# Kernel tuning notes

Measured on AMD Instinct MI355X. Metric: run time of the kernel, lower is better.

## Reference

```python
import jax, jax.numpy as jnp
import numpy as np

B, S, E, H = 4, 2048, 512, 1024

def setup_inputs() -> dict:
    key = jax.random.key(0)
    ks = jax.random.split(key, 8)
    s = 1.0 / np.sqrt(H)
    return {
        "hidden_states": jax.random.normal(ks[0], (B, S, H), jnp.float32),
        "external_embeddings": jax.random.normal(ks[1], (B, E, H), jnp.float32),
        "Wq": jax.random.normal(ks[2], (H, H), jnp.float32) * s,
        "bq": jax.random.normal(ks[3], (H,), jnp.float32) * 0.02,
        "Wk": jax.random.normal(ks[4], (H, H), jnp.float32) * s,
        "bk": jax.random.normal(ks[5], (H,), jnp.float32) * 0.02,
        "Wv": jax.random.normal(ks[6], (H, H), jnp.float32) * s,
        "bv": jax.random.normal(ks[7], (H,), jnp.float32) * 0.02,
    }

def reference(hidden_states, external_embeddings, Wq, bq, Wk, bk, Wv, bv):
    # Projections (torch Linear semantics: here weights stored as [in,out])
    q = hidden_states @ Wq + bq              # [B,S,H]
    k_tok = hidden_states @ Wk + bk          # [B,S,H]
    v_tok = hidden_states @ Wv + bv          # [B,S,H]
    k_ext = external_embeddings @ Wk + bk    # [B,E,H]
    v_ext = external_embeddings @ Wv + bv    # [B,E,H]
    # Each token attends to [its own key] ++ [external keys]; NO 1/sqrt(d) scaling
    # and NO head splitting, matching the original forward exactly.
    s_self = jnp.einsum('bsh,bsh->bs', q, k_tok)[..., None]   # [B,S,1]
    s_ext = jnp.einsum('bsh,beh->bse', q, k_ext)              # [B,S,E]
    scores = jnp.concatenate([s_self, s_ext], axis=-1)        # [B,S,1+E]
    probs = jax.nn.softmax(scores, axis=-1)
    ctx = probs[..., :1] * v_tok + jnp.einsum('bse,beh->bsh', probs[..., 1:], v_ext)
    return ctx  # [B,S,H]
```

## Files before the change

### kernel.cpp

```cpp
#include <hip/hip_runtime.h>
#include <stdint.h>

#define BB 4
#define SS 2048
#define EE 512
#define HH 1024

typedef _Float16 f16;
typedef __attribute__((ext_vector_type(8))) _Float16 f16x8;
typedef __attribute__((ext_vector_type(4))) _Float16 f16x4;
typedef __attribute__((ext_vector_type(4))) float f32x4;

__device__ __forceinline__ void async16(void* lds, const void* g) {
  __builtin_amdgcn_global_load_lds(
      (const __attribute__((address_space(1))) unsigned int*)g,
      (__attribute__((address_space(3))) unsigned int*)lds, 16, 0, 0);
}

#define MFMA16 __builtin_amdgcn_mfma_f32_16x16x32_f16

__global__ __launch_bounds__(256) void cast_kernel(const float* __restrict__ xh32,
                                                   const float* __restrict__ xe32,
                                                   f16* __restrict__ xh,
                                                   f16* __restrict__ xe) {
  const int i = blockIdx.x * 256 + threadIdx.x;
  const int n4h = 8192 * HH / 4;
  const float* src = i < n4h ? xh32 : xe32;
  f16* dst = i < n4h ? xh : xe;
  const int k = i < n4h ? i : i - n4h;
  const float4 v = ((const float4*)src)[k];
  f16x4 o;
  o.x = (f16)v.x; o.y = (f16)v.y; o.z = (f16)v.z; o.w = (f16)v.w;
  ((f16x4*)dst)[k] = o;
}

__global__ void wsplit_kernel(const float* __restrict__ Wq, const float* __restrict__ Wk,
                              const float* __restrict__ Wv, f16* __restrict__ wt_hi,
                              f16* __restrict__ wt_lo) {
  __shared__ float tile[32][33];
  const int k0 = blockIdx.x * 32;
  const int n0g = blockIdx.y * 32;
  const int which = n0g >> 10;
  const float* W = which == 0 ? Wq : (which == 1 ? Wk : Wv);
  const int n0 = n0g & 1023;
  const int tx = threadIdx.x, ty = threadIdx.y;
#pragma unroll
  for (int i = 0; i < 32; i += 8)
    tile[ty + i][tx] = W[(size_t)(k0 + ty + i) * 1024 + n0 + tx];
  __syncthreads();
#pragma unroll
  for (int i = 0; i < 32; i += 8) {
    const int np = n0g + ty + i;
    const float v = tile[tx][ty + i];
    const size_t idx = (size_t)np * 1024 + k0 + tx;
    const f16 h = (f16)v;
    wt_hi[idx] = h;
    wt_lo[idx] = (f16)(v - (float)h);
  }
}

__global__ __launch_bounds__(512, 2) void proj_kernel(
    const f16* __restrict__ xh, const f16* __restrict__ xe,
    const f16* __restrict__ wt_hi, const f16* __restrict__ wt_lo,
    const float* __restrict__ bq, const float* __restrict__ bk,
    const float* __restrict__ bv, f16* __restrict__ q_hi, f16* __restrict__ q_lo,
    f16* __restrict__ kt, f16* __restrict__ vt,
    f16* __restrict__ ke_hi, f16* __restrict__ ke_lo, f16* __restrict__ veT) {
  const int g = blockIdx.x;
  const int j = g & 7;
  const int s = g >> 3;
  int mrow0, colB0;
  bool ext = false, splitB = false;
  if (s < 20) {
    splitB = true;
    if (s < 16) {
      colB0 = (s >> 2) * 256;
      mrow0 = ((s & 3) * 8 + j) * 256;
    } else {
      ext = true;
      colB0 = 1024 + (s - 16) * 256;
      mrow0 = j * 256;
    }
  } else {
    const int s2 = s - 20;
    if (s2 < 32) {
      colB0 = (4 + (s2 >> 2)) * 256;
      mrow0 = ((s2 & 3) * 8 + j) * 256;
    } else {
      ext = true;
      colB0 = 1024 + (4 + (s2 - 32)) * 256;
      mrow0 = j * 256;
    }
  }
  const int NT = splitB ? 32 : 16;

  __shared__ f16 lds[65536];

  const int tid = threadIdx.x;
  const int wave = tid >> 6, lane = tid & 63;
  const int wm = wave >> 2, wn = wave & 3;
  const int frow = lane & 15, qd = lane >> 4;

  const f16* A0 = (ext ? xe : xh) + (size_t)mrow0 * HH;
  const f16* Bhi = wt_hi + (size_t)colB0 * HH;
  const f16* Blo = wt_lo + (size_t)colB0 * HH;

  const int srow = tid >> 2;
  const int scol = ((tid & 3) ^ ((srow >> 1) & 3)) * 8;
  const size_t gO0 = (size_t)srow * HH + scol;
  const size_t gO1 = (size_t)(128 + srow) * HH + scol;
  const int ldst0 = (wave * 64) * 8;
  const int ldst1 = (512 + wave * 64) * 8;

  int offA[8], offB[4];
#pragma unroll
  for (int i = 0; i < 8; ++i) {
    const int r = wm * 128 + i * 16 + frow;
    offA[i] = r * 32 + ((qd ^ ((r >> 1) & 3)) * 8);
  }
#pragma unroll
  for (int jj = 0; jj < 4; ++jj) {
    const int r = wn * 64 + jj * 16 + frow;
    offB[jj] = r * 32 + ((qd ^ ((r >> 1) & 3)) * 8);
  }

  f32x4 acc[8][4];
#pragma unroll
  for (int i = 0; i < 8; ++i)
#pragma unroll
    for (int jj = 0; jj < 4; ++jj)
#pragma unroll
      for (int r = 0; r < 4; ++r) acc[i][jj][r] = 0.0f;

  {
    f16* dA0 = &lds[0];
    f16* dB0 = &lds[32768];
    f16* dA1 = &lds[8192];
    f16* dB1 = &lds[32768 + 8192];
    async16(&dA0[ldst0], A0 + gO0);       async16(&dA0[ldst1], A0 + gO1);
    async16(&dB0[ldst0], Bhi + gO0);      async16(&dB0[ldst1], Bhi + gO1);
    async16(&dA1[ldst0], A0 + 32 + gO0);  async16(&dA1[ldst1], A0 + 32 + gO1);
    async16(&dB1[ldst0], Bhi + 32 + gO0); async16(&dB1[ldst1], Bhi + 32 + gO1);
  }
  asm volatile("s_waitcnt vmcnt(4)" ::: "memory");
  __builtin_amdgcn_s_barrier();

  for (int t = 0; t < NT; ++t) {
    const int cur = t & 1, nxt = cur ^ 1;
    const bool st = (t + 1 < NT);
    const int kn = ((t + 1) & 15) * 64;
    const f16* An = A0 + kn;
    const f16* Bn = (((t + 1) & 16) ? Blo : Bhi) + kn;
    const f16* lA0 = &lds[(cur * 2 + 0) * 8192];
    const f16* lB0 = &lds[32768 + (cur * 2 + 0) * 8192];
    const f16* lA1 = &lds[(cur * 2 + 1) * 8192];
    const f16* lB1 = &lds[32768 + (cur * 2 + 1) * 8192];
    f16* sA0 = &lds[(nxt * 2 + 0) * 8192];
    f16* sB0 = &lds[32768 + (nxt * 2 + 0) * 8192];
    f16* sA1 = &lds[(nxt * 2 + 1) * 8192];
    f16* sB1 = &lds[32768 + (nxt * 2 + 1) * 8192];

    f16x8 a[8], b0, b1;

#pragma unroll
    for (int i = 0; i < 8; ++i) a[i] = *(const f16x8*)&lA0[offA[i]];
    b0 = *(const f16x8*)&lB0[offB[0]];
    b1 = *(const f16x8*)&lB0[offB[1]];
    if (st) { async16(&sA0[ldst0], An + gO0); async16(&sA0[ldst1], An + gO1); }
    __builtin_amdgcn_s_barrier();
    __builtin_amdgcn_s_setprio(1);
#pragma unroll
    for (int i = 0; i < 8; ++i) {
      acc[i][0] = MFMA16(a[i], b0, acc[i][0], 0, 0, 0);
      acc[i][1] = MFMA16(a[i], b1, acc[i][1], 0, 0, 0);
    }
    __builtin_amdgcn_s_setprio(0);
    __builtin_amdgcn_s_barrier();

    b0 = *(const f16x8*)&lB0[offB[2]];
    b1 = *(const f16x8*)&lB0[offB[3]];
    if (st) { async16(&sB0[ldst0], Bn + gO0); async16(&sB0[ldst1], Bn + gO1); }
    __builtin_amdgcn_s_barrier();
    __builtin_amdgcn_s_setprio(1);
#pragma unroll
    for (int i = 0; i < 8; ++i) {
      acc[i][2] = MFMA16(a[i], b0, acc[i][2], 0, 0, 0);
      acc[i][3] = MFMA16(a[i], b1, acc[i][3], 0, 0, 0);
    }
    __builtin_amdgcn_s_setprio(0);
    if (t == NT - 1) {
      asm volatile("s_waitcnt vmcnt(0)" ::: "memory");
    } else {
      asm volatile("s_waitcnt vmcnt(4)" ::: "memory");
    }
    __builtin_amdgcn_s_barrier();

#pragma unroll
    for (int i = 0; i < 8; ++i) a[i] = *(const f16x8*)&lA1[offA[i]];
    b0 = *(const f16x8*)&lB1[offB[0]];
    b1 = *(const f16x8*)&lB1[offB[1]];
    if (st) { async16(&sA1[ldst0], An + 32 + gO0); async16(&sA1[ldst1], An + 32 + gO1); }
    __builtin_amdgcn_s_barrier();
    __builtin_amdgcn_s_setprio(1);
#pragma unroll
    for (int i = 0; i < 8; ++i) {
      acc[i][0] = MFMA16(a[i], b0, acc[i][0], 0, 0, 0);
      acc[i][1] = MFMA16(a[i], b1, acc[i][1], 0, 0, 0);
    }
    __builtin_amdgcn_s_setprio(0);
    __builtin_amdgcn_s_barrier();

    b0 = *(const f16x8*)&lB1[offB[2]];
    b1 = *(const f16x8*)&lB1[offB[3]];
    if (st) { async16(&sB1[ldst0], Bn + 32 + gO0); async16(&sB1[ldst1], Bn + 32 + gO1); }
    __builtin_amdgcn_s_barrier();
    __builtin_amdgcn_s_setprio(1);
#pragma unroll
    for (int i = 0; i < 8; ++i) {
      acc[i][2] = MFMA16(a[i], b0, acc[i][2], 0, 0, 0);
      acc[i][3] = MFMA16(a[i], b1, acc[i][3], 0, 0, 0);
    }
    __builtin_amdgcn_s_setprio(0);
    asm volatile("s_waitcnt vmcnt(4)" ::: "memory");
    __builtin_amdgcn_s_barrier();
  }

  const int er0 = wm * 128 + qd * 4;
  const int ec0 = wn * 64 + frow;
  float bias[4];
#pragma unroll
  for (int jj = 0; jj < 4; ++jj) {
    const int c = colB0 + ec0 + jj * 16;
    bias[jj] = c < 1024 ? bq[c] : (c < 2048 ? bk[c - 1024] : bv[c - 2048]);
  }

  if (!ext) {
    if (colB0 < 1024) {
#pragma unroll
      for (int jj = 0; jj < 4; ++jj) {
        const int c = colB0 + ec0 + jj * 16;
#pragma unroll
        for (int i = 0; i < 8; ++i)
#pragma unroll
          for (int r = 0; r < 4; ++r) {
            const int row = mrow0 + er0 + i * 16 + r;
            const float val = acc[i][jj][r] + bias[jj];
            const size_t idx = (size_t)row * HH + c;
            const f16 h = (f16)val;
            q_hi[idx] = h;
            q_lo[idx] = (f16)(val - (float)h);
          }
      }
    } else if (colB0 < 2048) {
#pragma unroll
      for (int jj = 0; jj < 4; ++jj) {
        const int c = colB0 + ec0 + jj * 16 - 1024;
#pragma unroll
        for (int i = 0; i < 8; ++i)
#pragma unroll
          for (int r = 0; r < 4; ++r) {
            const int row = mrow0 + er0 + i * 16 + r;
            kt[(size_t)row * HH + c] = (f16)(acc[i][jj][r] + bias[jj]);
          }
      }
    } else {
#pragma unroll
      for (int jj = 0; jj < 4; ++jj) {
        const int c = colB0 + ec0 + jj * 16 - 2048;
#pragma unroll
        for (int i = 0; i < 8; ++i)
#pragma unroll
          for (int r = 0; r < 4; ++r) {
            const int row = mrow0 + er0 + i * 16 + r;
            vt[(size_t)row * HH + c] = (f16)(acc[i][jj][r] + bias[jj]);
          }
      }
    }
  } else {
    if (colB0 < 2048) {
#pragma unroll
      for (int jj = 0; jj < 4; ++jj) {
        const int c = colB0 + ec0 + jj * 16 - 1024;
#pragma unroll
        for (int i = 0; i < 8; ++i)
#pragma unroll
          for (int r = 0; r < 4; ++r) {
            const int row = mrow0 + er0 + i * 16 + r;
            const float val = acc[i][jj][r] + bias[jj];
            const size_t idx = (size_t)row * HH + c;
            const f16 h = (f16)val;
            ke_hi[idx] = h;
            ke_lo[idx] = (f16)(val - (float)h);
          }
      }
    } else {
      f16* tl = lds;
      const int b = mrow0 >> 9, e0 = mrow0 & 511;
      const int h0 = colB0 - 2048;
#pragma unroll
      for (int p = 0; p < 2; ++p) {
        __syncthreads();
        if ((wn >> 1) == p) {
          const int hL = (wn & 1) * 64 + frow;
#pragma unroll
          for (int jj = 0; jj < 4; ++jj)
#pragma unroll
            for (int i = 0; i < 8; ++i)
#pragma unroll
              for (int r = 0; r < 4; ++r) {
                const int e = er0 + i * 16 + r;
                tl[(hL + jj * 16) * 264 + e] = (f16)(acc[i][jj][r] + bias[jj]);
              }
        }
        __syncthreads();
        for (int c = tid; c < 128 * 32; c += 512) {
          const int hL = c >> 5, ch = c & 31;
          const f16x8 v = *(const f16x8*)&tl[hL * 264 + ch * 8];
          *(f16x8*)&veT[(size_t)(b * HH + h0 + p * 128 + hL) * EE + e0 + ch * 8] = v;
        }
      }
    }
  }
}

__global__ __launch_bounds__(512, 1) void score_kernel(
    const f16* __restrict__ q_hi, const f16* __restrict__ q_lo,
    const f16* __restrict__ ke_hi, const f16* __restrict__ ke_lo,
    float* __restrict__ s_part) {
  const int b = blockIdx.z & 3;
  const int khalf = blockIdx.z >> 2;
  const int mtile = blockIdx.y;
  const int ntile = blockIdx.x;

  __shared__ f16 lds[73728];

  const int tid = threadIdx.x;
  const int wave = tid >> 6, lane = tid & 63;
  const int wm = wave >> 1, wn = wave & 1;
  const int frow = lane & 15, qd = lane >> 4;

  const size_t aoff = ((size_t)b * SS + mtile * 256) * HH + khalf * 512;
  const size_t boff = ((size_t)b * EE + ntile * 128) * HH + khalf * 512;
  const f16* Ah = q_hi + aoff;
  const f16* Al = q_lo + aoff;
  const f16* Bh = ke_hi + boff;
  const f16* Bl = ke_lo + boff;

  const int srow = tid >> 2;
  const int scol = ((tid & 3) ^ ((srow >> 1) & 3)) * 8;
  const size_t gA0 = (size_t)srow * HH + scol;
  const size_t gA1 = (size_t)(128 + srow) * HH + scol;
  const int ldstA0 = (wave * 64) * 8;
  const int ldstA1 = (512 + wave * 64) * 8;
  const int ldstB0 = (wave * 64) * 8;

  int offA[4], offB[4];
#pragma unroll
  for (int i = 0; i < 4; ++i) {
    const int r = wm * 64 + i * 16 + frow;
    offA[i] = r * 32 + ((qd ^ ((r >> 1) & 3)) * 8);
  }
#pragma unroll
  for (int jj = 0; jj < 4; ++jj) {
    const int r = wn * 64 + jj * 16 + frow;
    offB[jj] = r * 32 + ((qd ^ ((r >> 1) & 3)) * 8);
  }

  f32x4 acc[4][4];
#pragma unroll
  for (int i = 0; i < 4; ++i)
#pragma unroll
    for (int jj = 0; jj < 4; ++jj)
#pragma unroll
      for (int r = 0; r < 4; ++r) acc[i][jj][r] = 0.0f;

#pragma unroll
  for (int p = 0; p < 2; ++p) {
    f16* dAh = &lds[p * 24576];
    f16* dAl = &lds[p * 24576 + 8192];
    f16* dBh = &lds[p * 24576 + 16384];
    f16* dBl = &lds[p * 24576 + 20480];
    const int ko = p * 32;
    async16(&dAh[ldstA0], Ah + ko + gA0); async16(&dAh[ldstA1], Ah + ko + gA1);
    async16(&dBh[ldstB0], Bh + ko + gA0);
    async16(&dBl[ldstB0], Bl + ko + gA0);
    async16(&dAl[ldstA0], Al + ko + gA0); async16(&dAl[ldstA1], Al + ko + gA1);
  }
  asm volatile("s_waitcnt vmcnt(6)" ::: "memory");
  __builtin_amdgcn_s_barrier();

  int cur = 0, stg = 2;
  for (int t = 0; t < 16; ++t) {
    const bool st = (t < 14);
    const int kk = (t + 2) * 32;
    const f16* lAh = &lds[cur * 24576];
    const f16* lAl = &lds[cur * 24576 + 8192];
    const f16* lBh = &lds[cur * 24576 + 16384];
    const f16* lBl = &lds[cur * 24576 + 20480];
    f16* sAh = &lds[stg * 24576];
    f16* sAl = &lds[stg * 24576 + 8192];
    f16* sBh = &lds[stg * 24576 + 16384];
    f16* sBl = &lds[stg * 24576 + 20480];

    f16x8 ah[4], bh[4], x[4];

#pragma unroll
    for (int i = 0; i < 4; ++i) ah[i] = *(const f16x8*)&lAh[offA[i]];
#pragma unroll
    for (int jj = 0; jj < 4; ++jj) bh[jj] = *(const f16x8*)&lBh[offB[jj]];
    if (st) {
      async16(&sAh[ldstA0], Ah + kk + gA0); async16(&sAh[ldstA1], Ah + kk + gA1);
    }
    __builtin_amdgcn_s_barrier();
    __builtin_amdgcn_s_setprio(1);
#pragma unroll
    for (int i = 0; i < 4; ++i)
#pragma unroll
      for (int jj = 0; jj < 4; ++jj)
        acc[i][jj] = MFMA16(ah[i], bh[jj], acc[i][jj], 0, 0, 0);
    __builtin_amdgcn_s_setprio(0);
    __builtin_amdgcn_s_barrier();

#pragma unroll
    for (int jj = 0; jj < 4; ++jj) x[jj] = *(const f16x8*)&lBl[offB[jj]];
    if (st) {
      async16(&sBh[ldstB0], Bh + kk + gA0);
      async16(&sBl[ldstB0], Bl + kk + gA0);
    }
    __builtin_amdgcn_s_barrier();
    __builtin_amdgcn_s_setprio(1);
#pragma unroll
    for (int i = 0; i < 4; ++i)
#pragma unroll
      for (int jj = 0; jj < 4; ++jj)
        acc[i][jj] = MFMA16(ah[i], x[jj], acc[i][jj], 0, 0, 0);
    __builtin_amdgcn_s_setprio(0);
    __builtin_amdgcn_s_barrier();

#pragma unroll
    for (int i = 0; i < 4; ++i) x[i] = *(const f16x8*)&lAl[offA[i]];
    if (st) {
      async16(&sAl[ldstA0], Al + kk + gA0); async16(&sAl[ldstA1], Al + kk + gA1);
    }
    __builtin_amdgcn_s_barrier();
    __builtin_amdgcn_s_setprio(1);
#pragma unroll
    for (int i = 0; i < 4; ++i)
#pragma unroll
      for (int jj = 0; jj < 4; ++jj)
        acc[i][jj] = MFMA16(x[i], bh[jj], acc[i][jj], 0, 0, 0);
    __builtin_amdgcn_s_setprio(0);
    if (t < 14)       { asm volatile("s_waitcnt vmcnt(6)" ::: "memory"); }
    else if (t == 14) { asm volatile("s_waitcnt vmcnt(0)" ::: "memory"); }
    __builtin_amdgcn_s_barrier();

    cur = (cur == 2) ? 0 : cur + 1;
    stg = (stg == 2) ? 0 : stg + 1;
  }

  float* dst = s_part + (size_t)khalf * BB * SS * EE + (size_t)b * SS * EE;
#pragma unroll
  for (int jj = 0; jj < 4; ++jj) {
    const int e = ntile * 128 + wn * 64 + jj * 16 + frow;
#pragma unroll
    for (int i = 0; i < 4; ++i)
#pragma unroll
      for (int r = 0; r < 4; ++r) {
        const int s = mtile * 256 + wm * 64 + i * 16 + qd * 4 + r;
        dst[(size_t)s * EE + e] = acc[i][jj][r];
      }
  }
}

__global__ __launch_bounds__(256) void softmax_kernel(
    const f16* __restrict__ q_hi, const f16* __restrict__ q_lo,
    const f16* __restrict__ kt, const float* __restrict__ s_part,
    f16* __restrict__ probs, float* __restrict__ p_self) {
  const int t = blockIdx.x * 4 + (threadIdx.x >> 6);
  const int lane = threadIdx.x & 63;

  const size_t base = (size_t)t * HH;
  float ss = 0.f;
#pragma unroll
  for (int it = 0; it < 4; ++it) {
    const int off = it * 256 + lane * 4;
    const f16x4 qh = *(const f16x4*)&q_hi[base + off];
    const f16x4 ql = *(const f16x4*)&q_lo[base + off];
    const f16x4 kh = *(const f16x4*)&kt[base + off];
    ss += ((float)qh.x + (float)ql.x) * (float)kh.x;
    ss += ((float)qh.y + (float)ql.y) * (float)kh.y;
    ss += ((float)qh.z + (float)ql.z) * (float)kh.z;
    ss += ((float)qh.w + (float)ql.w) * (float)kh.w;
  }
#pragma unroll
  for (int m = 32; m > 0; m >>= 1) ss += __shfl_xor(ss, m, 64);

  const float* r0 = s_part + (size_t)t * EE;
  const float* r1 = s_part + (size_t)BB * SS * EE + (size_t)t * EE;
  const float4 a0 = *(const float4*)&r0[lane * 4];
  const float4 a1 = *(const float4*)&r0[256 + lane * 4];
  const float4 c0 = *(const float4*)&r1[lane * 4];
  const float4 c1 = *(const float4*)&r1[256 + lane * 4];
  const float v0x = a0.x + c0.x, v0y = a0.y + c0.y, v0z = a0.z + c0.z, v0w = a0.w + c0.w;
  const float v1x = a1.x + c1.x, v1y = a1.y + c1.y, v1z = a1.z + c1.z, v1w = a1.w + c1.w;
  float m = fmaxf(fmaxf(fmaxf(v0x, v0y), fmaxf(v0z, v0w)),
                  fmaxf(fmaxf(v1x, v1y), fmaxf(v1z, v1w)));
#pragma unroll
  for (int sh = 32; sh > 0; sh >>= 1) m = fmaxf(m, __shfl_xor(m, sh, 64));
  m = fmaxf(m, ss);
  const float e0 = __expf(v0x - m), e1 = __expf(v0y - m);
  const float e2 = __expf(v0z - m), e3 = __expf(v0w - m);
  const float e4 = __expf(v1x - m), e5 = __expf(v1y - m);
  const float e6 = __expf(v1z - m), e7 = __expf(v1w - m);
  float sum = ((e0 + e1) + (e2 + e3)) + ((e4 + e5) + (e6 + e7));
#pragma unroll
  for (int sh = 32; sh > 0; sh >>= 1) sum += __shfl_xor(sum, sh, 64);
  const float es = __expf(ss - m);
  const float inv = 1.0f / (sum + es);
  f16x4 p0, p1;
  p0.x = (f16)(e0 * inv); p0.y = (f16)(e1 * inv);
  p0.z = (f16)(e2 * inv); p0.w = (f16)(e3 * inv);
  p1.x = (f16)(e4 * inv); p1.y = (f16)(e5 * inv);
  p1.z = (f16)(e6 * inv); p1.w = (f16)(e7 * inv);
  *(f16x4*)&probs[(size_t)t * EE + lane * 4] = p0;
  *(f16x4*)&probs[(size_t)t * EE + 256 + lane * 4] = p1;
  if (lane == 0) p_self[t] = es * inv;
}

__global__ __launch_bounds__(512, 2) void pv_kernel(
    const f16* __restrict__ probs, const f16* __restrict__ veT,
    const float* __restrict__ p_self, const f16* __restrict__ vt,
    float* __restrict__ out) {
  const int b = blockIdx.z;
  const int mtile = blockIdx.y;
  const int ntile = blockIdx.x;

  __shared__ f16 lds[36864];

  const int tid = threadIdx.x;
  const int wave = tid >> 6, lane = tid & 63;
  const int wm = wave >> 1, wn = wave & 1;
  const int frow = lane & 15, qd = lane >> 4;

  const size_t aoff = ((size_t)b * SS + mtile * 256) * EE;
  const size_t boff = ((size_t)b * HH + ntile * 128) * EE;
  const f16* A = probs + aoff;
  const f16* Bv = veT + boff;

  const int srow = tid >> 2;
  const int scol = ((tid & 3) ^ ((srow >> 1) & 3)) * 8;
  const size_t gA0 = (size_t)srow * EE + scol;
  const size_t gA1 = (size_t)(128 + srow) * EE + scol;
  const int ldstA0 = (wave * 64) * 8;
  const int ldstA1 = (512 + wave * 64) * 8;
  const int ldstB0 = (wave * 64) * 8;

  int offA[4], offB[4];
#pragma unroll
  for (int i = 0; i < 4; ++i) {
    const int r = wm * 64 + i * 16 + frow;
    offA[i] = r * 32 + ((qd ^ ((r >> 1) & 3)) * 8);
  }
#pragma unroll
  for (int jj = 0; jj < 4; ++jj) {
    const int r = wn * 64 + jj * 16 + frow;
    offB[jj] = r * 32 + ((qd ^ ((r >> 1) & 3)) * 8);
  }

  f32x4 acc[4][4];
#pragma unroll
  for (int i = 0; i < 4; ++i)
#pragma unroll
    for (int jj = 0; jj < 4; ++jj)
#pragma unroll
      for (int r = 0; r < 4; ++r) acc[i][jj][r] = 0.0f;

  {
    f16* dA0 = &lds[0], *dB0 = &lds[8192];
    f16* dA1 = &lds[12288], *dB1 = &lds[12288 + 8192];
    async16(&dA0[ldstA0], A + gA0); async16(&dA0[ldstA1], A + gA1);
    async16(&dB0[ldstB0], Bv + gA0);
    async16(&dA1[ldstA0], A + 32 + gA0); async16(&dA1[ldstA1], A + 32 + gA1);
    async16(&dB1[ldstB0], Bv + 32 + gA0);
  }
  asm volatile("s_waitcnt vmcnt(3)" ::: "memory");
  __builtin_amdgcn_s_barrier();

  int cur = 0, stg = 2;
  for (int t = 0; t < 16; ++t) {
    const bool st = (t < 14);
    const int kk = (t + 2) * 32;
    const f16* lA = &lds[cur * 12288];
    const f16* lB = &lds[cur * 12288 + 8192];
    f16* sA = &lds[stg * 12288];
    f16* sB = &lds[stg * 12288 + 8192];

    f16x8 a[4], b[4];

#pragma unroll
    for (int i = 0; i < 4; ++i) a[i] = *(const f16x8*)&lA[offA[i]];
    b[0] = *(const f16x8*)&lB[offB[0]];
    b[1] = *(const f16x8*)&lB[offB[1]];
    if (st) { async16(&sA[ldstA0], A + kk + gA0); async16(&sA[ldstA1], A + kk + gA1); }
    __builtin_amdgcn_s_barrier();
    __builtin_amdgcn_s_setprio(1);
#pragma unroll
    for (int i = 0; i < 4; ++i) {
      acc[i][0] = MFMA16(a[i], b[0], acc[i][0], 0, 0, 0);
      acc[i][1] = MFMA16(a[i], b[1], acc[i][1], 0, 0, 0);
    }
    __builtin_amdgcn_s_setprio(0);
    __builtin_amdgcn_s_barrier();

    b[2] = *(const f16x8*)&lB[offB[2]];
    b[3] = *(const f16x8*)&lB[offB[3]];
    if (st) async16(&sB[ldstB0], Bv + kk + gA0);
    __builtin_amdgcn_s_barrier();
    __builtin_amdgcn_s_setprio(1);
#pragma unroll
    for (int i = 0; i < 4; ++i) {
      acc[i][2] = MFMA16(a[i], b[2], acc[i][2], 0, 0, 0);
      acc[i][3] = MFMA16(a[i], b[3], acc[i][3], 0, 0, 0);
    }
    __builtin_amdgcn_s_setprio(0);
    if (t < 14)      { asm volatile("s_waitcnt vmcnt(3)" ::: "memory"); }
    else if (t == 14){ asm volatile("s_waitcnt vmcnt(0)" ::: "memory"); }
    __builtin_amdgcn_s_barrier();

    cur = (cur == 2) ? 0 : cur + 1;
    stg = (stg == 2) ? 0 : stg + 1;
  }

#pragma unroll
  for (int jj = 0; jj < 4; ++jj) {
    const int h = ntile * 128 + wn * 64 + jj * 16 + frow;
#pragma unroll
    for (int i = 0; i < 4; ++i)
#pragma unroll
      for (int r = 0; r < 4; ++r) {
        const int s = mtile * 256 + wm * 64 + i * 16 + qd * 4 + r;
        const size_t t = (size_t)b * SS + s;
        __builtin_nontemporal_store(
            acc[i][jj][r] + p_self[t] * (float)vt[t * HH + h], &out[t * HH + h]);
      }
  }
}

extern "C" void kernel_launch(void* const* d_in, const int* in_sizes, int n_in,
                              void* d_out, int out_size, void* d_ws, size_t ws_size,
                              hipStream_t stream) {
  const float* hidden = (const float*)d_in[0];
  const float* ext    = (const float*)d_in[1];
  const float* Wq = (const float*)d_in[2];
  const float* bq = (const float*)d_in[3];
  const float* Wk = (const float*)d_in[4];
  const float* bk = (const float*)d_in[5];
  const float* Wv = (const float*)d_in[6];
  const float* bv = (const float*)d_in[7];
  float* out = (float*)d_out;

  char* ws = (char*)d_ws;
  size_t off = 0;
  auto alloc = [&](size_t bytes) {
    char* p = ws + off;
    off += (bytes + 255) & ~(size_t)255;
    return p;
  };
  const size_t TOK = 8192, EXT = 2048;
  f16* xh    = (f16*)alloc(TOK * HH * 2);
  f16* xe    = (f16*)alloc(EXT * HH * 2);
  f16* wt_hi = (f16*)alloc(3072ull * HH * 2);
  f16* wt_lo = (f16*)alloc(3072ull * HH * 2);
  f16* q_hi  = (f16*)alloc(TOK * HH * 2);
  f16* q_lo  = (f16*)alloc(TOK * HH * 2);
  f16* kt    = (f16*)alloc(TOK * HH * 2);
  f16* vt    = (f16*)alloc(TOK * HH * 2);
  f16* ke_hi = (f16*)alloc(EXT * HH * 2);
  f16* ke_lo = (f16*)alloc(EXT * HH * 2);
  f16* veT   = (f16*)alloc((size_t)BB * HH * EE * 2);
  float* p_self = (float*)alloc(TOK * 4);
  float* s_part = (float*)alloc(2ull * BB * SS * EE * 4);
  f16* probs    = (f16*)alloc((size_t)BB * SS * EE * 2);

  cast_kernel<<<10240, 256, 0, stream>>>(hidden, ext, xh, xe);
  wsplit_kernel<<<dim3(32, 96), dim3(32, 8), 0, stream>>>(Wq, Wk, Wv, wt_hi, wt_lo);

  proj_kernel<<<448, 512, 0, stream>>>(
      xh, xe, wt_hi, wt_lo, bq, bk, bv,
      q_hi, q_lo, kt, vt, ke_hi, ke_lo, veT);

  score_kernel<<<dim3(4, 8, 8), 512, 0, stream>>>(q_hi, q_lo, ke_hi, ke_lo, s_part);
  softmax_kernel<<<2048, 256, 0, stream>>>(q_hi, q_lo, kt, s_part, probs, p_self);
  pv_kernel<<<dim3(8, 8, 4), 512, 0, stream>>>(probs, veT, p_self, vt, out);
}
```

Before: 282.8 us.

## Merge prep kernels and simplify projection GEMM pipeline to smaller K-steps

Fuses the input cast kernel and the weight split/transpose kernel into one launch, removing one kernel launch. The projection GEMM now uses a 32-wide K-step with a plain double buffer: one async prefetch per iteration, a vmcnt(0) wait and one barrier, replacing the four-phase 64-wide schedule with many barriers. LDS use is halved, launch bounds are raised to 4 blocks per CU, and the veT transpose epilogue is reworked to fit the smaller LDS. In exchange it waits for each load to fully drain every step, and the tighter register budget risks spilling the 128-float accumulator.

```diff
diff --git a/kernel.cpp b/kernel.cpp
--- a/kernel.cpp
+++ b/kernel.cpp
@@ -19,47 +19,49 @@
 
 #define MFMA16 __builtin_amdgcn_mfma_f32_16x16x32_f16
 
-__global__ __launch_bounds__(256) void cast_kernel(const float* __restrict__ xh32,
-                                                   const float* __restrict__ xe32,
-                                                   f16* __restrict__ xh,
-                                                   f16* __restrict__ xe) {
-  const int i = blockIdx.x * 256 + threadIdx.x;
-  const int n4h = 8192 * HH / 4;
-  const float* src = i < n4h ? xh32 : xe32;
-  f16* dst = i < n4h ? xh : xe;
-  const int k = i < n4h ? i : i - n4h;
-  const float4 v = ((const float4*)src)[k];
-  f16x4 o;
-  o.x = (f16)v.x; o.y = (f16)v.y; o.z = (f16)v.z; o.w = (f16)v.w;
-  ((f16x4*)dst)[k] = o;
+__global__ __launch_bounds__(256) void prep_kernel(
+    const float* __restrict__ xh32, const float* __restrict__ xe32,
+    const float* __restrict__ Wq, const float* __restrict__ Wk,
+    const float* __restrict__ Wv,
+    f16* __restrict__ xh, f16* __restrict__ xe,
+    f16* __restrict__ wt_hi, f16* __restrict__ wt_lo) {
+  __shared__ float tile[32][33];
+  const int bid = blockIdx.x;
+  if (bid < 10240) {
+    const int i = bid * 256 + threadIdx.x;
+    const int n4h = 8192 * HH / 4;
+    const float* src = i < n4h ? xh32 : xe32;
+    f16* dst = i < n4h ? xh : xe;
+    const int k = i < n4h ? i : i - n4h;
+    const float4 v = ((const float4*)src)[k];
+    f16x4 o;
+    o.x = (f16)v.x; o.y = (f16)v.y; o.z = (f16)v.z; o.w = (f16)v.w;
+    ((f16x4*)dst)[k] = o;
+  } else {
+    const int b2 = bid - 10240;
+    const int k0 = (b2 & 31) * 32;
+    const int n0g = (b2 >> 5) * 32;
+    const int which = n0g >> 10;
+    const float* W = which == 0 ? Wq : (which == 1 ? Wk : Wv);
+    const int n0 = n0g & 1023;
+    const int tx = threadIdx.x & 31, ty = threadIdx.x >> 5;
+#pragma unroll
+    for (int i = 0; i < 32; i += 8)
+      tile[ty + i][tx] = W[(size_t)(k0 + ty + i) * 1024 + n0 + tx];
+    __syncthreads();
+#pragma unroll
+    for (int i = 0; i < 32; i += 8) {
+      const int np = n0g + ty + i;
+      const float v = tile[tx][ty + i];
+      const size_t idx = (size_t)np * 1024 + k0 + tx;
+      const f16 h = (f16)v;
+      wt_hi[idx] = h;
+      wt_lo[idx] = (f16)(v - (float)h);
+    }
+  }
 }
 
-__global__ void wsplit_kernel(const float* __restrict__ Wq, const float* __restrict__ Wk,
-                              const float* __restrict__ Wv, f16* __restrict__ wt_hi,
-                              f16* __restrict__ wt_lo) {
-  __shared__ float tile[32][33];
-  const int k0 = blockIdx.x * 32;
-  const int n0g = blockIdx.y * 32;
-  const int which = n0g >> 10;
-  const float* W = which == 0 ? Wq : (which == 1 ? Wk : Wv);
-  const int n0 = n0g & 1023;
-  const int tx = threadIdx.x, ty = threadIdx.y;
-#pragma unroll
-  for (int i = 0; i < 32; i += 8)
-    tile[ty + i][tx] = W[(size_t)(k0 + ty + i) * 1024 + n0 + tx];
-  __syncthreads();
-#pragma unroll
-  for (int i = 0; i < 32; i += 8) {
-    const int np = n0g + ty + i;
-    const float v = tile[tx][ty + i];
-    const size_t idx = (size_t)np * 1024 + k0 + tx;
-    const f16 h = (f16)v;
-    wt_hi[idx] = h;
-    wt_lo[idx] = (f16)(v - (float)h);
-  }
-}
-
-__global__ __launch_bounds__(512, 2) void proj_kernel(
+__global__ __launch_bounds__(512, 4) void proj_kernel(
     const f16* __restrict__ xh, const f16* __restrict__ xe,
     const f16* __restrict__ wt_hi, const f16* __restrict__ wt_lo,
     const float* __restrict__ bq, const float* __restrict__ bk,
@@ -92,9 +94,9 @@
       mrow0 = j * 256;
     }
   }
-  const int NT = splitB ? 32 : 16;
-
-  __shared__ f16 lds[65536];
+  const int NT = splitB ? 64 : 32;
+
+  __shared__ f16 lds[32768];
 
   const int tid = threadIdx.x;
   const int wave = tid >> 6, lane = tid & 63;
@@ -109,8 +111,8 @@
   const int scol = ((tid & 3) ^ ((srow >> 1) & 3)) * 8;
   const size_t gO0 = (size_t)srow * HH + scol;
   const size_t gO1 = (size_t)(128 + srow) * HH + scol;
-  const int ldst0 = (wave * 64) * 8;
-  const int ldst1 = (512 + wave * 64) * 8;
+  const int ldst0 = wave * 512;
+  const int ldst1 = 4096 + wave * 512;
 
   int offA[8], offB[4];
 #pragma unroll
@@ -132,42 +134,32 @@
 #pragma unroll
       for (int r = 0; r < 4; ++r) acc[i][jj][r] = 0.0f;
 
-  {
-    f16* dA0 = &lds[0];
-    f16* dB0 = &lds[32768];
-    f16* dA1 = &lds[8192];
-    f16* dB1 = &lds[32768 + 8192];
-    async16(&dA0[ldst0], A0 + gO0);       async16(&dA0[ldst1], A0 + gO1);
-    async16(&dB0[ldst0], Bhi + gO0);      async16(&dB0[ldst1], Bhi + gO1);
-    async16(&dA1[ldst0], A0 + 32 + gO0);  async16(&dA1[ldst1], A0 + 32 + gO1);
-    async16(&dB1[ldst0], Bhi + 32 + gO0); async16(&dB1[ldst1], Bhi + 32 + gO1);
-  }
-  asm volatile("s_waitcnt vmcnt(4)" ::: "memory");
+  async16(&lds[ldst0], A0 + gO0);        async16(&lds[ldst1], A0 + gO1);
+  async16(&lds[8192 + ldst0], Bhi + gO0); async16(&lds[8192 + ldst1], Bhi + gO1);
+  asm volatile("s_waitcnt vmcnt(0)" ::: "memory");
   __builtin_amdgcn_s_barrier();
 
   for (int t = 0; t < NT; ++t) {
     const int cur = t & 1, nxt = cur ^ 1;
-    const bool st = (t + 1 < NT);
-    const int kn = ((t + 1) & 15) * 64;
-    const f16* An = A0 + kn;
-    const f16* Bn = (((t + 1) & 16) ? Blo : Bhi) + kn;
-    const f16* lA0 = &lds[(cur * 2 + 0) * 8192];
-    const f16* lB0 = &lds[32768 + (cur * 2 + 0) * 8192];
-    const f16* lA1 = &lds[(cur * 2 + 1) * 8192];
-    const f16* lB1 = &lds[32768 + (cur * 2 + 1) * 8192];
-    f16* sA0 = &lds[(nxt * 2 + 0) * 8192];
-    f16* sB0 = &lds[32768 + (nxt * 2 + 0) * 8192];
-    f16* sA1 = &lds[(nxt * 2 + 1) * 8192];
-    f16* sB1 = &lds[32768 + (nxt * 2 + 1) * 8192];
+    const f16* bufA = &lds[cur * 16384];
+    const f16* bufB = &lds[cur * 16384 + 8192];
+    f16* sA = &lds[nxt * 16384];
+    f16* sB = &lds[nxt * 16384 + 8192];
+
+    if (t + 1 < NT) {
+      const int ks = t + 1;
+      const int ko = (ks & 31) * 32;
+      const f16* As = A0 + ko;
+      const f16* Bs = ((splitB && ks >= 32) ? Blo : Bhi) + ko;
+      async16(&sA[ldst0], As + gO0); async16(&sA[ldst1], As + gO1);
+      async16(&sB[ldst0], Bs + gO0); async16(&sB[ldst1], Bs + gO1);
+    }
 
     f16x8 a[8], b0, b1;
-
-#pragma unroll
-    for (int i = 0; i < 8; ++i) a[i] = *(const f16x8*)&lA0[offA[i]];
-    b0 = *(const f16x8*)&lB0[offB[0]];
-    b1 = *(const f16x8*)&lB0[offB[1]];
-    if (st) { async16(&sA0[ldst0], An + gO0); async16(&sA0[ldst1], An + gO1); }
-    __builtin_amdgcn_s_barrier();
+#pragma unroll
+    for (int i = 0; i < 8; ++i) a[i] = *(const f16x8*)&bufA[offA[i]];
+    b0 = *(const f16x8*)&bufB[offB[0]];
+    b1 = *(const f16x8*)&bufB[offB[1]];
     __builtin_amdgcn_s_setprio(1);
 #pragma unroll
     for (int i = 0; i < 8; ++i) {
@@ -175,12 +167,8 @@
       acc[i][1] = MFMA16(a[i], b1, acc[i][1], 0, 0, 0);
     }
     __builtin_amdgcn_s_setprio(0);
-    __builtin_amdgcn_s_barrier();
-
-    b0 = *(const f16x8*)&lB0[offB[2]];
-    b1 = *(const f16x8*)&lB0[offB[3]];
-    if (st) { async16(&sB0[ldst0], Bn + gO0); async16(&sB0[ldst1], Bn + gO1); }
-    __builtin_amdgcn_s_barrier();
+    b0 = *(const f16x8*)&bufB[offB[2]];
+    b1 = *(const f16x8*)&bufB[offB[3]];
     __builtin_amdgcn_s_setprio(1);
 #pragma unroll
     for (int i = 0; i < 8; ++i) {
@@ -188,40 +176,7 @@
       acc[i][3] = MFMA16(a[i], b1, acc[i][3], 0, 0, 0);
     }
     __builtin_amdgcn_s_setprio(0);
-    if (t == NT - 1) {
-      asm volatile("s_waitcnt vmcnt(0)" ::: "memory");
-    } else {
-      asm volatile("s_waitcnt vmcnt(4)" ::: "memory");
-    }
-    __builtin_amdgcn_s_barrier();
-
-#pragma unroll
-    for (int i = 0; i < 8; ++i) a[i] = *(const f16x8*)&lA1[offA[i]];
-    b0 = *(const f16x8*)&lB1[offB[0]];
-    b1 = *(const f16x8*)&lB1[offB[1]];
-    if (st) { async16(&sA1[ldst0], An + 32 + gO0); async16(&sA1[ldst1], An + 32 + gO1); }
-    __builtin_amdgcn_s_barrier();
-    __builtin_amdgcn_s_setprio(1);
-#pragma unroll
-    for (int i = 0; i < 8; ++i) {
-      acc[i][0] = MFMA16(a[i], b0, acc[i][0], 0, 0, 0);
-      acc[i][1] = MFMA16(a[i], b1, acc[i][1], 0, 0, 0);
-    }
-    __builtin_amdgcn_s_setprio(0);
-    __builtin_amdgcn_s_barrier();
-
-    b0 = *(const f16x8*)&lB1[offB[2]];
-    b1 = *(const f16x8*)&lB1[offB[3]];
-    if (st) { async16(&sB1[ldst0], Bn + 32 + gO0); async16(&sB1[ldst1], Bn + 32 + gO1); }
-    __builtin_amdgcn_s_barrier();
-    __builtin_amdgcn_s_setprio(1);
-#pragma unroll
-    for (int i = 0; i < 8; ++i) {
-      acc[i][2] = MFMA16(a[i], b0, acc[i][2], 0, 0, 0);
-      acc[i][3] = MFMA16(a[i], b1, acc[i][3], 0, 0, 0);
-    }
-    __builtin_amdgcn_s_setprio(0);
-    asm volatile("s_waitcnt vmcnt(4)" ::: "memory");
+    asm volatile("s_waitcnt vmcnt(0)" ::: "memory");
     __builtin_amdgcn_s_barrier();
   }
 
@@ -298,10 +253,10 @@
       const int b = mrow0 >> 9, e0 = mrow0 & 511;
       const int h0 = colB0 - 2048;
 #pragma unroll
-      for (int p = 0; p < 2; ++p) {
+      for (int p = 0; p < 4; ++p) {
         __syncthreads();
-        if ((wn >> 1) == p) {
-          const int hL = (wn & 1) * 64 + frow;
+        if (wn == p) {
+          const int hL = frow;
 #pragma unroll
           for (int jj = 0; jj < 4; ++jj)
 #pragma unroll
@@ -313,10 +268,10 @@
               }
         }
         __syncthreads();
-        for (int c = tid; c < 128 * 32; c += 512) {
+        for (int c = tid; c < 64 * 32; c += 512) {
           const int hL = c >> 5, ch = c & 31;
           const f16x8 v = *(const f16x8*)&tl[hL * 264 + ch * 8];
-          *(f16x8*)&veT[(size_t)(b * HH + h0 + p * 128 + hL) * EE + e0 + ch * 8] = v;
+          *(f16x8*)&veT[(size_t)(b * HH + h0 + p * 64 + hL) * EE + e0 + ch * 8] = v;
         }
       }
     }
@@ -682,8 +637,8 @@
   float* s_part = (float*)alloc(2ull * BB * SS * EE * 4);
   f16* probs    = (f16*)alloc((size_t)BB * SS * EE * 2);
 
-  cast_kernel<<<10240, 256, 0, stream>>>(hidden, ext, xh, xe);
-  wsplit_kernel<<<dim3(32, 96), dim3(32, 8), 0, stream>>>(Wq, Wk, Wv, wt_hi, wt_lo);
+  prep_kernel<<<13312, 256, 0, stream>>>(hidden, ext, Wq, Wk, Wv,
+                                         xh, xe, wt_hi, wt_lo);
 
   proj_kernel<<<448, 512, 0, stream>>>(
       xh, xe, wt_hi, wt_lo, bq, bk, bv,
```

Measured after the change: 939.3 us. +232.1%, slower.
